# Performance work log

Measured on AMD Instinct MI355X. Metric: run time of the kernel, lower is better.

Reference implementation:

```python
import jax, jax.numpy as jnp
import numpy as np

N = 12000   # nodes (multiple of 120)
E = 192000  # edges
T = 120     # utterances per dialogue
IN = 192
OUT = 6


def _edge_softmax(logits, dst, n):
    # logits: [E, H] -> softmax over incoming edges of each dst node
    m = jax.ops.segment_max(logits, dst, num_segments=n)
    ex = jnp.exp(logits - m[dst])
    s = jax.ops.segment_sum(ex, dst, num_segments=n)
    return ex / s[dst]


def _gatv2(h, src, dst, Wsrc, bsrc, Wdst, bdst, attn, Wres, n):
    # DGL GATv2Conv: e = attn . leakyrelu(fc_src(h)[u] + fc_dst(h)[v]), residual, relu activation
    Hh, F = attn.shape
    fs = (h @ Wsrc + bsrc).reshape(n, Hh, F)
    fd = (h @ Wdst + bdst).reshape(n, Hh, F)
    e = jax.nn.leaky_relu(fs[src] + fd[dst], 0.2)          # [E, H, F]
    logits = jnp.einsum('ehf,hf->eh', e, attn)              # [E, H]
    alpha = _edge_softmax(logits, dst, n)                   # [E, H]
    out = jax.ops.segment_sum(alpha[:, :, None] * fs[src], dst, num_segments=n)
    res = (h @ Wres).reshape(n, Hh, F)
    return jax.nn.relu(out + res)                           # [N, H, F]


def _lstm_dir(x, Wih, Whh, bih, bhh, reverse):
    # x: [T, B, D]; torch gate order i, f, g, o
    B = x.shape[1]
    hid = Whh.shape[1]
    def step(carry, xt):
        h, c = carry
        z = xt @ Wih.T + h @ Whh.T + bih + bhh
        i, f, g, o = jnp.split(z, 4, axis=-1)
        c = jax.nn.sigmoid(f) * c + jax.nn.sigmoid(i) * jnp.tanh(g)
        h = jax.nn.sigmoid(o) * jnp.tanh(c)
        return (h, c), h
    init = (jnp.zeros((B, hid), x.dtype), jnp.zeros((B, hid), x.dtype))
    _, hs = jax.lax.scan(step, init, x, reverse=reverse)
    return hs


def setup_inputs() -> dict:
    key = jax.random.key(0)
    ks = iter(jax.random.split(key, 64))
    def rn(shape, s=0.05):
        return jax.random.normal(next(ks), shape, jnp.float32) * s
    inp = {
        'text': rn((N, 1024), 1.0),
        'audio': rn((N, 512), 1.0),
        'vision': rn((N, 1024), 1.0),
        'edge_src': jax.random.randint(next(ks), (E,), 0, N, jnp.int32),
        'edge_dst': jax.random.randint(next(ks), (E,), 0, N, jnp.int32),
        # modality encoders
        'W_audio': rn((512, 64)), 'b_audio': jnp.zeros((64,), jnp.float32),
        'W_vision': rn((1024, 64)), 'b_vision': jnp.zeros((64,), jnp.float32),
        'W_text': rn((1024, 64)), 'b_text': jnp.zeros((64,), jnp.float32),
        # bidirectional LSTM (hidden=4 -> 16 gate rows)
        'Wih_f': rn((16, IN)), 'Whh_f': rn((16, 4)), 'bih_f': jnp.zeros((16,), jnp.float32), 'bhh_f': jnp.zeros((16,), jnp.float32),
        'Wih_b': rn((16, IN)), 'Whh_b': rn((16, 4)), 'bih_b': jnp.zeros((16,), jnp.float32), 'bhh_b': jnp.zeros((16,), jnp.float32),
        # imputation GraphConv (192->192, norm='both')
        'W_gc': rn((IN, IN)), 'b_gc': jnp.zeros((IN,), jnp.float32),
        # gat2 (cross-modal multi-head GAT, 192 -> 16 heads x 4)
        'Wsrc2': rn((IN, 64)), 'bsrc2': jnp.zeros((64,), jnp.float32),
        'Wdst2': rn((IN, 64)), 'bdst2': jnp.zeros((64,), jnp.float32),
        'attn2': rn((16, 4)), 'Wres2': rn((IN, 64)),
        # gat1 layer 0 (192 -> 16 heads x 32)
        'Wsrc0': rn((IN, 512)), 'bsrc0': jnp.zeros((512,), jnp.float32),
        'Wdst0': rn((IN, 512)), 'bdst0': jnp.zeros((512,), jnp.float32),
        'attn0': rn((16, 32)), 'Wres0': rn((IN, 512)),
        # gat1 layer 1 (512 -> 16 heads x 4)
        'Wsrc1': rn((512, 64)), 'bsrc1': jnp.zeros((64,), jnp.float32),
        'Wdst1': rn((512, 64)), 'bdst1': jnp.zeros((64,), jnp.float32),
        'attn1': rn((16, 4)), 'Wres1': rn((512, 64)),
        # final classifier Linear(136, out_size)
        'W_lin': rn((136, OUT)), 'b_lin': jnp.zeros((OUT,), jnp.float32),
    }
    return inp


def reference(text, audio, vision, edge_src, edge_dst,
              W_audio, b_audio, W_vision, b_vision, W_text, b_text,
              Wih_f, Whh_f, bih_f, bhh_f, Wih_b, Whh_b, bih_b, bhh_b,
              W_gc, b_gc,
              Wsrc2, bsrc2, Wdst2, bdst2, attn2, Wres2,
              Wsrc0, bsrc0, Wdst0, bdst0, attn0, Wres0,
              Wsrc1, bsrc1, Wdst1, bdst1, attn1, Wres1,
              W_lin, b_lin):
    n = text.shape[0]
    # modality encoders (dropout is identity at inference)
    t = text @ W_text + b_text
    a = audio @ W_audio + b_audio
    v = vision @ W_vision + b_vision
    stackFT = jnp.concatenate([t, a, v], axis=1)            # [N, 192]

    # bidirectional LSTM over dialogues of length T=120
    x = stackFT.reshape(-1, T, IN).transpose(1, 0, 2)       # [T, B, 192]
    hf = _lstm_dir(x, Wih_f, Whh_f, bih_f, bhh_f, False)
    hb = _lstm_dir(x, Wih_b, Whh_b, bih_b, bhh_b, True)
    newFeature = jnp.concatenate([hf, hb], -1).transpose(1, 0, 2).reshape(n, 8)

    # GraphConv imputation, norm='both' (degrees clamped to 1 as in DGL)
    ones = jnp.ones((edge_src.shape[0],), stackFT.dtype)
    deg_out = jnp.maximum(jax.ops.segment_sum(ones, edge_src, num_segments=n), 1.0)
    deg_in = jnp.maximum(jax.ops.segment_sum(ones, edge_dst, num_segments=n), 1.0)
    hw = (stackFT @ W_gc) * (deg_out ** -0.5)[:, None]
    h1 = jax.ops.segment_sum(hw[edge_src], edge_dst, num_segments=n) * (deg_in ** -0.5)[:, None] + b_gc
    h = 0.5 * (stackFT + h1)
    # F.normalize(h, p=1)
    h = h / jnp.maximum(jnp.sum(jnp.abs(h), axis=1, keepdims=True), 1e-12)

    # cross-modal multi-head GAT branch -> [N, 64]
    h3 = _gatv2(h, edge_src, edge_dst, Wsrc2, bsrc2, Wdst2, bdst2, attn2, Wres2, n).reshape(n, -1)

    # stacked GATv2 layers
    h = _gatv2(h, edge_src, edge_dst, Wsrc0, bsrc0, Wdst0, bdst0, attn0, Wres0, n).reshape(n, -1)  # [N, 512]
    h = _gatv2(h, edge_src, edge_dst, Wsrc1, bsrc1, Wdst1, bdst1, attn1, Wres1, n).reshape(n, -1)  # [N, 64]

    out = jnp.concatenate([h, newFeature, h3], axis=1) @ W_lin + b_lin  # [N, out_size]
    return out
```

## Files before the change

### kernel.cpp

```cpp
#include <hip/hip_runtime.h>

typedef __attribute__((ext_vector_type(8))) short short8;
typedef __attribute__((ext_vector_type(4))) float f32x4;
typedef _Float16 half8v __attribute__((ext_vector_type(8)));

__device__ __forceinline__ unsigned short f2bf(float f) {
    unsigned u = __float_as_uint(f);
    u += 0x7FFFu + ((u >> 16) & 1u);
    return (unsigned short)(u >> 16);
}
__device__ __forceinline__ float bf2f(unsigned short h) {
    return __uint_as_float((unsigned)h << 16);
}

template<int MF, int OUTMODE>
__global__ __launch_bounds__(256)
void gemm_v7(const unsigned short* __restrict__ A, const unsigned short* __restrict__ B,
             const float* __restrict__ bias, const float* __restrict__ rowscale,
             void* __restrict__ Cv, const float* __restrict__ fin_num,
             const float* __restrict__ fin_den,
             int M, int Nb, int K, int ldc)
{
    __shared__ alignas(16) unsigned short As[MF * 64 * 32];
    __shared__ alignas(16) unsigned short Bs[4 * 64 * 8];
    const int t = threadIdx.x;
    const int w = t >> 6, l = t & 63;
    const int r16 = l & 15, kg = l >> 4;
    const int row0 = blockIdx.x * (64 * MF);
    const int col0 = blockIdx.y * 64;
    const int bcol = t & 63, bkg = t >> 6;

    f32x4 acc[MF][4] = {};
    const short8 z8 = {0, 0, 0, 0, 0, 0, 0, 0};

    int srow[MF], sch[MF];
    bool va[MF];
    const unsigned short* aptr[MF];
#pragma unroll
    for (int it = 0; it < MF; ++it) {
        int idx = it * 256 + t;
        srow[it] = idx >> 2; sch[it] = idx & 3;
        int gm = row0 + srow[it];
        va[it] = gm < M;
        aptr[it] = A + (size_t)gm * K + sch[it] * 8;
    }
    const unsigned short* bptr = B + (size_t)(bkg * 8) * Nb + col0 + bcol;

    short8 pa[MF];
    unsigned short pbv[8];
#pragma unroll
    for (int it = 0; it < MF; ++it)
        pa[it] = va[it] ? *reinterpret_cast<const short8*>(aptr[it]) : z8;
#pragma unroll
    for (int j = 0; j < 8; ++j) pbv[j] = bptr[(size_t)j * Nb];

    for (int k0 = 0; k0 < K; k0 += 32) {
#pragma unroll
        for (int it = 0; it < MF; ++it)
            *reinterpret_cast<short8*>(&As[srow[it] * 32 + sch[it] * 8]) = pa[it];
        {
            short8 hv;
#pragma unroll
            for (int j = 0; j < 8; ++j) hv[j] = (short)pbv[j];
            *reinterpret_cast<short8*>(&Bs[bkg * 512 + bcol * 8]) = hv;
        }
        __syncthreads();
        if (k0 + 32 < K) {
#pragma unroll
            for (int it = 0; it < MF; ++it)
                pa[it] = va[it] ? *reinterpret_cast<const short8*>(aptr[it] + k0 + 32) : z8;
#pragma unroll
            for (int j = 0; j < 8; ++j) pbv[j] = bptr[(size_t)(k0 + 32 + j) * Nb];
        }
        short8 af[MF];
#pragma unroll
        for (int mi = 0; mi < MF; ++mi)
            af[mi] = *reinterpret_cast<const short8*>(&As[((w * MF + mi) * 16 + r16) * 32 + kg * 8]);
#pragma unroll
        for (int ni = 0; ni < 4; ++ni) {
            short8 bf = *reinterpret_cast<const short8*>(&Bs[kg * 512 + (ni * 16 + r16) * 8]);
#pragma unroll
            for (int mi = 0; mi < MF; ++mi)
                acc[mi][ni] = __builtin_amdgcn_mfma_f32_16x16x32_bf16(af[mi], bf, acc[mi][ni], 0, 0, 0);
        }
        __syncthreads();
    }
#pragma unroll
    for (int mi = 0; mi < MF; ++mi)
#pragma unroll
        for (int ni = 0; ni < 4; ++ni) {
            int col = col0 + ni * 16 + r16;
            float bv = bias ? bias[col] : 0.f;
#pragma unroll
            for (int r = 0; r < 4; ++r) {
                int gm = row0 + (w * MF + mi) * 16 + kg * 4 + r;
                if (gm < M) {
                    float val = acc[mi][ni][r] + bv;
                    if (rowscale) val *= rowscale[gm];
                    size_t idx = (size_t)gm * ldc + col;
                    if (OUTMODE == 0) {
                        ((float*)Cv)[idx] = val;
                    } else if (OUTMODE == 1) {
                        ((unsigned short*)Cv)[idx] = f2bf(val);
                    } else {
                        float d = fin_den[(size_t)gm * 16 + (col >> 5)];
                        float inv = (d > 0.f) ? __fdividef(1.f, d) : 0.f;
                        float o = fmaxf(fin_num[idx] * inv + val, 0.f);
                        ((unsigned short*)Cv)[idx] = f2bf(o);
                    }
                }
            }
        }
}

__global__ __launch_bounds__(256)
void enc_f16v6(const float* __restrict__ text, const float* __restrict__ audio, const float* __restrict__ vision,
               const _Float16* __restrict__ Wf16,
               const float* __restrict__ bt, const float* __restrict__ ba, const float* __restrict__ bv,
               float* __restrict__ Cf, unsigned short* __restrict__ Cb, int M)
{
    __shared__ float tbuf[4][16][68];
    const int gw = (blockIdx.x * blockDim.x + threadIdx.x) >> 6;
    const int wib = threadIdx.x >> 6;
    const int l = threadIdx.x & 63;
    const int tpm = M >> 4;
    if (gw >= 3 * tpm) return;
    const int z = gw / tpm;
    const int tidx = gw - z * tpm;
    const float* A  = (z == 0) ? text : (z == 1) ? audio : vision;
    const _Float16* Wp = Wf16 + ((z == 0) ? 0 : (z == 1) ? 65536 : 98304) + l * 8;
    const float* bb = (z == 0) ? bt : (z == 1) ? ba : bv;
    const int KC = (z == 1) ? 16 : 32;

    const float* ap = A + (size_t)(tidx * 16 + (l & 15)) * (KC * 32) + (l >> 4) * 8;

    f32x4 acc0 = {}, acc1 = {}, acc2 = {}, acc3 = {};
    float4 na0 = *reinterpret_cast<const float4*>(ap);
    float4 na1 = *reinterpret_cast<const float4*>(ap + 4);
    half8v nb0 = *reinterpret_cast<const half8v*>(Wp);
    half8v nb1 = *reinterpret_cast<const half8v*>(Wp + 512);
    half8v nb2 = *reinterpret_cast<const half8v*>(Wp + 1024);
    half8v nb3 = *reinterpret_cast<const half8v*>(Wp + 1536);

    for (int kc = 0; kc < KC; ++kc) {
        float4 ca0 = na0, ca1 = na1;
        half8v cb0 = nb0, cb1 = nb1, cb2 = nb2, cb3 = nb3;
        if (kc + 1 < KC) {
            const float* apn = ap + (kc + 1) * 32;
            na0 = *reinterpret_cast<const float4*>(apn);
            na1 = *reinterpret_cast<const float4*>(apn + 4);
            const _Float16* wpn = Wp + (size_t)(kc + 1) * 2048;
            nb0 = *reinterpret_cast<const half8v*>(wpn);
            nb1 = *reinterpret_cast<const half8v*>(wpn + 512);
            nb2 = *reinterpret_cast<const half8v*>(wpn + 1024);
            nb3 = *reinterpret_cast<const half8v*>(wpn + 1536);
        }
        half8v af;
        af[0] = (_Float16)ca0.x; af[1] = (_Float16)ca0.y;
        af[2] = (_Float16)ca0.z; af[3] = (_Float16)ca0.w;
        af[4] = (_Float16)ca1.x; af[5] = (_Float16)ca1.y;
        af[6] = (_Float16)ca1.z; af[7] = (_Float16)ca1.w;
        acc0 = __builtin_amdgcn_mfma_f32_16x16x32_f16(af, cb0, acc0, 0, 0, 0);
        acc1 = __builtin_amdgcn_mfma_f32_16x16x32_f16(af, cb1, acc1, 0, 0, 0);
        acc2 = __builtin_amdgcn_mfma_f32_16x16x32_f16(af, cb2, acc2, 0, 0, 0);
        acc3 = __builtin_amdgcn_mfma_f32_16x16x32_f16(af, cb3, acc3, 0, 0, 0);
    }

    const int r16 = l & 15, hi = l >> 4;
    float* tl = &tbuf[wib][0][0];
#pragma unroll
    for (int cg = 0; cg < 4; ++cg) {
        f32x4 a = (cg == 0) ? acc0 : (cg == 1) ? acc1 : (cg == 2) ? acc2 : acc3;
        int col = cg * 16 + r16;
        float bvv = bb[col];
#pragma unroll
        for (int r = 0; r < 4; ++r)
            tl[(hi * 4 + r) * 68 + col] = a[r] + bvv;
    }
#pragma unroll
    for (int r = 0; r < 16; ++r) {
        float val = tl[r * 68 + l];
        size_t idx = (size_t)(tidx * 16 + r) * 192 + z * 64 + l;
        Cf[idx] = val;
        Cb[idx] = f2bf(val);
    }
}

__global__ void pack_all(const float* __restrict__ Wt, const float* __restrict__ Wa, const float* __restrict__ Wv,
                         const float* __restrict__ Wgc,
                         const float* __restrict__ Ws2, const float* __restrict__ Wd2, const float* __restrict__ Wr2,
                         const float* __restrict__ bs2, const float* __restrict__ bd2,
                         const float* __restrict__ Ws0, const float* __restrict__ Wd0,
                         const float* __restrict__ bs0, const float* __restrict__ bd0,
                         const float* __restrict__ Wr0,
                         const float* __restrict__ Ws1, const float* __restrict__ Wd1, const float* __restrict__ Wr1,
                         const float* __restrict__ bs1, const float* __restrict__ bd1,
                         _Float16* __restrict__ encW, unsigned short* __restrict__ Wall, float* __restrict__ ball)
{
    int gid = blockIdx.x * blockDim.x + threadIdx.x;
    if (gid < 163840) {
        const float* Wsrcp;
        int base;
        if (gid < 65536)      { base = 0;     Wsrcp = Wt; }
        else if (gid < 98304) { base = 65536; Wsrcp = Wa; }
        else                  { base = 98304; Wsrcp = Wv; }
        int i = gid - base;
        int kc = i >> 11, r = i & 2047;
        int cg = r >> 9, lane = (r >> 3) & 63, j = r & 7;
        int k = kc * 32 + (lane >> 4) * 8 + j;
        int col = cg * 16 + (lane & 15);
        encW[gid] = (_Float16)Wsrcp[k * 64 + col];
    }
    if (gid < 36864) {
        Wall[gid] = f2bf(Wgc[gid]);
    } else if (gid < 73728) {
        int i = gid - 36864, k = i / 192, c = i - k * 192;
        float v = (c < 64) ? Ws2[k * 64 + c] : (c < 128) ? Wd2[k * 64 + c - 64] : Wr2[k * 64 + c - 128];
        Wall[gid] = f2bf(v);
    } else if (gid < 270336) {
        int i = gid - 73728, k = i >> 10, c = i & 1023;
        float v = (c < 512) ? Ws0[k * 512 + c] : Wd0[k * 512 + c - 512];
        Wall[gid] = f2bf(v);
    } else if (gid < 368640) {
        Wall[gid] = f2bf(Wr0[gid - 270336]);
    } else if (gid < 466944) {
        int i = gid - 368640, k = i / 192, c = i - k * 192;
        float v = (c < 64) ? Ws1[k * 64 + c] : (c < 128) ? Wd1[k * 64 + c - 64] : Wr1[k * 64 + c - 128];
        Wall[gid] = f2bf(v);
    } else if (gid < 468352) {
        int i = gid - 466944;
        float v;
        if (i < 192)       v = (i < 64) ? bs2[i] : (i < 128) ? bd2[i - 64] : 0.f;
        else if (i < 1216) { int j = i - 192; v = (j < 512) ? bs0[j] : bd0[j - 512]; }
        else               { int j = i - 1216; v = (j < 64) ? bs1[j] : (j < 128) ? bd1[j - 64] : 0.f; }
        ball[i] = v;
    }
}

__global__ void deg_kernel(const int* __restrict__ src, const int* __restrict__ dst,
                           int* degout, int* degin, int E)
{
    int e = blockIdx.x * blockDim.x + threadIdx.x;
    if (e < E) {
        atomicAdd(&degout[src[e]], 1);
        atomicAdd(&degin[dst[e]], 1);
    }
}

__global__ __launch_bounds__(1024)
void scan_kernel(const int* __restrict__ degin, const int* __restrict__ degout,
                 int* __restrict__ rowstart, float* __restrict__ rso, float* __restrict__ rsi, int n)
{
    __shared__ int part[1024];
    int t = threadIdx.x;
    int chunk = (n + 1023) / 1024;
    int s = 0;
    for (int i = 0; i < chunk; ++i) {
        int idx = t * chunk + i;
        if (idx < n) s += degin[idx];
    }
    part[t] = s;
    __syncthreads();
    for (int o = 1; o < 1024; o <<= 1) {
        int v = (t >= o) ? part[t - o] : 0;
        __syncthreads();
        part[t] += v;
        __syncthreads();
    }
    int run = (t > 0) ? part[t - 1] : 0;
    for (int i = 0; i < chunk; ++i) {
        int idx = t * chunk + i;
        if (idx < n) {
            rowstart[idx] = run; run += degin[idx];
            rso[idx] = rsqrtf((float)max(degout[idx], 1));
            rsi[idx] = rsqrtf((float)max(degin[idx], 1));
        }
    }
    if (t == 1023) rowstart[n] = part[1023];
}

__global__ void perm_kernel(const int* __restrict__ dst, const int* __restrict__ rowstart,
                            int* cursor, int* __restrict__ perm, int E)
{
    int e = blockIdx.x * blockDim.x + threadIdx.x;
    if (e < E) {
        int v = dst[e];
        int p = atomicAdd(&cursor[v], 1);
        perm[rowstart[v] + p] = e;
    }
}

__global__ void gather_src_kernel(const int* __restrict__ esrc, int* perm, int E)
{
    int i = blockIdx.x * blockDim.x + threadIdx.x;
    if (i < E) perm[i] = esrc[perm[i]];
}

__global__ void lstm_pre(const float* __restrict__ x, const float* __restrict__ Wf,
                         const float* __restrict__ Wb,
                         const float* bf1, const float* bf2, const float* bb1, const float* bb2,
                         float* __restrict__ xWf, float* __restrict__ xWb, int n)
{
    int gid = blockIdx.x * blockDim.x + threadIdx.x;
    if (gid >= n * 32) return;
    int nn = gid >> 5, r = gid & 31, d = r >> 4, j = r & 15;
    const float* W = (d ? Wb : Wf) + j * 192;
    const float* xr = x + (size_t)nn * 192;
    float s = 0.f;
#pragma unroll 4
    for (int k = 0; k < 192; k += 4) {
        float4 xv = *reinterpret_cast<const float4*>(xr + k);
        float4 wv = *reinterpret_cast<const float4*>(W + k);
        s += xv.x * wv.x + xv.y * wv.y + xv.z * wv.z + xv.w * wv.w;
    }
    s += d ? (bb1[j] + bb2[j]) : (bf1[j] + bf2[j]);
    int b = nn / 120, tt = nn - b * 120;
    (d ? xWb : xWf)[((size_t)b * 16 + j) * 120 + tt] = s;
}

__device__ __forceinline__ float fsigm(float x) { return __fdividef(1.f, 1.f + __expf(-x)); }
__device__ __forceinline__ float ftanh(float x) { return 1.f - __fdividef(2.f, __expf(2.f * x) + 1.f); }

template<int DIR>
__device__ void lstm_chain(const float* __restrict__ xw, const float* __restrict__ whh,
                           float* __restrict__ newF, int b)
{
    int j = threadIdx.x & 15;
    int k = j & 3;
    float4 w = *reinterpret_cast<const float4*>(whh + j * 4);
    const float* xp = xw + ((size_t)b * 16 + j) * 120;
    float h0 = 0.f, h1 = 0.f, h2 = 0.f, h3 = 0.f, cst = 0.f;
    int tb0 = DIR ? 108 : 0;
    float4 a0 = *reinterpret_cast<const float4*>(xp + tb0);
    float4 a1 = *reinterpret_cast<const float4*>(xp + tb0 + 4);
    float4 a2 = *reinterpret_cast<const float4*>(xp + tb0 + 8);
    for (int ch = 0; ch < 10; ++ch) {
        float4 b0 = a0, b1 = a1, b2 = a2;
        if (ch < 9) {
            int nt = DIR ? (96 - ch * 12) : (12 + ch * 12);
            b0 = *reinterpret_cast<const float4*>(xp + nt);
            b1 = *reinterpret_cast<const float4*>(xp + nt + 4);
            b2 = *reinterpret_cast<const float4*>(xp + nt + 8);
        }
        float zz[12] = {a0.x, a0.y, a0.z, a0.w, a1.x, a1.y, a1.z, a1.w, a2.x, a2.y, a2.z, a2.w};
        int tbase = DIR ? (108 - ch * 12) : (ch * 12);
#pragma unroll
        for (int ii = 0; ii < 12; ++ii) {
            int idx = DIR ? (11 - ii) : ii;
            float z = zz[idx] + ((w.x * h0 + w.y * h1) + (w.z * h2 + w.w * h3));
            float zi = __shfl(z, k, 16);
            float zf = __shfl(z, k + 4, 16);
            float zg = __shfl(z, k + 8, 16);
            float zo = __shfl(z, k + 12, 16);
            float ig = fsigm(zi), fg = fsigm(zf), gg = ftanh(zg), og = fsigm(zo);
            cst = fg * cst + ig * gg;
            float hn = og * ftanh(cst);
            h0 = __shfl(hn, 0, 16); h1 = __shfl(hn, 1, 16);
            h2 = __shfl(hn, 2, 16); h3 = __shfl(hn, 3, 16);
            if (j < 4) newF[((size_t)b * 120 + tbase + idx) * 8 + DIR * 4 + j] = hn;
        }
        a0 = b0; a1 = b1; a2 = b2;
    }
}

__global__ __launch_bounds__(64)
void lstm_seq2(const float* __restrict__ xWf, const float* __restrict__ xWb,
               const float* __restrict__ Whhf, const float* __restrict__ Whhb,
               float* __restrict__ newF, int B)
{
    int sub = threadIdx.x >> 4;
    int chain = blockIdx.x * 4 + sub;
    if (chain >= 2 * B) return;
    int d = chain / B;
    int b = chain - d * B;
    if (d == 0) lstm_chain<0>(xWf, Whhf, newF, b);
    else        lstm_chain<1>(xWb, Whhb, newF, b);
}

__global__ __launch_bounds__(256)
void gc_combine5(const float* __restrict__ stackFT, const unsigned short* __restrict__ hw,
                 const int* __restrict__ rowstart, const int* __restrict__ csrc,
                 const float* __restrict__ rs_in,
                 const float* __restrict__ b_gc, unsigned short* __restrict__ hB, int n)
{
    int v = blockIdx.x * 4 + (threadIdx.x >> 6);
    int l = threadIdx.x & 63;
    if (v >= n) return;
    int s0 = rowstart[v], s1 = rowstart[v + 1];
    float sum0 = 0.f, sum1 = 0.f, sum2 = 0.f;

    unsigned short a0 = 0, a1 = 0, a2 = 0, b0 = 0, b1 = 0, b2 = 0;
    auto LD = [&](int i, unsigned short& x0, unsigned short& x1, unsigned short& x2) {
        const unsigned short* hr = hw + (size_t)csrc[i] * 192 + l;
        x0 = hr[0]; x1 = hr[64]; x2 = hr[128];
    };
    int i = s0;
    if (i < s1) LD(i, a0, a1, a2);
    if (i + 1 < s1) LD(i + 1, b0, b1, b2);
    for (; i + 2 < s1; i += 2) {
        unsigned short n0, n1, n2, m0 = 0, m1 = 0, m2 = 0;
        LD(i + 2, n0, n1, n2);
        if (i + 3 < s1) LD(i + 3, m0, m1, m2);
        sum0 += bf2f(a0) + bf2f(b0);
        sum1 += bf2f(a1) + bf2f(b1);
        sum2 += bf2f(a2) + bf2f(b2);
        a0 = n0; a1 = n1; a2 = n2; b0 = m0; b1 = m1; b2 = m2;
    }
    if (i < s1) { sum0 += bf2f(a0); sum1 += bf2f(a1); sum2 += bf2f(a2); }
    if (i + 1 < s1) { sum0 += bf2f(b0); sum1 += bf2f(b1); sum2 += bf2f(b2); }

    float ri = rs_in[v];
    const float* sf = stackFT + (size_t)v * 192 + l;
    float v0 = 0.5f * (sf[0]   + sum0 * ri + b_gc[l]);
    float v1 = 0.5f * (sf[64]  + sum1 * ri + b_gc[l + 64]);
    float v2 = 0.5f * (sf[128] + sum2 * ri + b_gc[l + 128]);
    float r = fabsf(v0) + fabsf(v1) + fabsf(v2);
#pragma unroll
    for (int o = 32; o; o >>= 1) r += __shfl_xor(r, o);
    float inv = __fdividef(1.f, fmaxf(r, 1e-12f));
    unsigned short* hp = hB + (size_t)v * 192 + l;
    hp[0]   = f2bf(v0 * inv);
    hp[64]  = f2bf(v1 * inv);
    hp[128] = f2bf(v2 * inv);
}

__global__ __launch_bounds__(256)
void gat_edge4c(const unsigned short* __restrict__ base,
                const float* __restrict__ attn,
                const int* __restrict__ rowstart, const int* __restrict__ csrc,
                float* __restrict__ outp, int n)
{
    int v = blockIdx.x * 16 + (threadIdx.x >> 4);
    int l = threadIdx.x & 15;
    if (v >= n) return;
    float4 at = *reinterpret_cast<const float4*>(attn + l * 4);
    ushort4 fdu = *reinterpret_cast<const ushort4*>(base + (size_t)v * 192 + 64 + l * 4);
    float fd0 = bf2f(fdu.x), fd1 = bf2f(fdu.y), fd2 = bf2f(fdu.z), fd3 = bf2f(fdu.w);
    float ac0 = 0.f, ac1 = 0.f, ac2 = 0.f, ac3 = 0.f, dn = 0.f;
    int s0 = rowstart[v], s1 = rowstart[v + 1];

    auto LD = [&](int i) -> ushort4 {
        return *reinterpret_cast<const ushort4*>(base + (size_t)csrc[i] * 192 + l * 4);
    };
    auto ACC = [&](ushort4 su) {
        float s0f = bf2f(su.x), s1f = bf2f(su.y), s2f = bf2f(su.z), s3f = bf2f(su.w);
        float e0 = s0f + fd0; e0 = fmaxf(e0, 0.2f * e0);
        float e1 = s1f + fd1; e1 = fmaxf(e1, 0.2f * e1);
        float e2 = s2f + fd2; e2 = fmaxf(e2, 0.2f * e2);
        float e3 = s3f + fd3; e3 = fmaxf(e3, 0.2f * e3);
        float p = e0 * at.x + e1 * at.y + e2 * at.z + e3 * at.w;
        float ex = __expf(p);
        ac0 += ex * s0f; ac1 += ex * s1f; ac2 += ex * s2f; ac3 += ex * s3f;
        dn += ex;
    };
    const ushort4 zu = make_ushort4(0, 0, 0, 0);
    ushort4 c0 = zu, c1 = zu;
    int i = s0;
    if (i < s1) c0 = LD(i);
    if (i + 1 < s1) c1 = LD(i + 1);
    for (; i + 2 < s1; i += 2) {
        ushort4 n0 = LD(i + 2);
        ushort4 n1 = (i + 3 < s1) ? LD(i + 3) : zu;
        ACC(c0); ACC(c1);
        c0 = n0; c1 = n1;
    }
    if (i < s1) ACC(c0);
    if (i + 1 < s1) ACC(c1);

    ushort4 ru = *reinterpret_cast<const ushort4*>(base + (size_t)v * 192 + 128 + l * 4);
    float inv = (dn > 0.f) ? __fdividef(1.f, dn) : 0.f;
    float4 o;
    o.x = fmaxf(ac0 * inv + bf2f(ru.x), 0.f);
    o.y = fmaxf(ac1 * inv + bf2f(ru.y), 0.f);
    o.z = fmaxf(ac2 * inv + bf2f(ru.z), 0.f);
    o.w = fmaxf(ac3 * inv + bf2f(ru.w), 0.f);
    *reinterpret_cast<float4*>(outp + (size_t)v * 64 + l * 4) = o;
}

__global__ __launch_bounds__(256)
void gat_edge32b(const unsigned short* __restrict__ base,
                 const float* __restrict__ attn,
                 const int* __restrict__ rowstart, const int* __restrict__ csrc,
                 float* __restrict__ num, float* __restrict__ den, int n)
{
    int v = blockIdx.x * 4 + (threadIdx.x >> 6);
    int l = threadIdx.x & 63;
    if (v >= n) return;
    float at[8];
    {
        float4 aA = *reinterpret_cast<const float4*>(attn + l * 8);
        float4 aB = *reinterpret_cast<const float4*>(attn + l * 8 + 4);
        at[0] = aA.x; at[1] = aA.y; at[2] = aA.z; at[3] = aA.w;
        at[4] = aB.x; at[5] = aB.y; at[6] = aB.z; at[7] = aB.w;
    }
    float fd[8];
    {
        short8 fdu = *reinterpret_cast<const short8*>(base + (size_t)v * 1024 + 512 + l * 8);
#pragma unroll
        for (int j = 0; j < 8; ++j) fd[j] = bf2f((unsigned short)fdu[j]);
    }
    float acc[8] = {};
    float dn = 0.f;
    int s0 = rowstart[v], s1 = rowstart[v + 1];

    auto LD = [&](int i) -> short8 {
        return *reinterpret_cast<const short8*>(base + (size_t)csrc[i] * 1024 + l * 8);
    };
    auto ACC = [&](short8 su) {
        float sf[8];
        float p = 0.f;
#pragma unroll
        for (int j = 0; j < 8; ++j) {
            sf[j] = bf2f((unsigned short)su[j]);
            float e = sf[j] + fd[j];
            e = fmaxf(e, 0.2f * e);
            p += e * at[j];
        }
        p += __shfl_xor(p, 1, 4);
        p += __shfl_xor(p, 2, 4);
        float ex = __expf(p);
#pragma unroll
        for (int j = 0; j < 8; ++j) acc[j] += ex * sf[j];
        dn += ex;
    };
    const short8 z8 = {0, 0, 0, 0, 0, 0, 0, 0};
    short8 c0 = z8, c1 = z8;
    int i = s0;
    if (i < s1) c0 = LD(i);
    if (i + 1 < s1) c1 = LD(i + 1);
    for (; i + 2 < s1; i += 2) {
        short8 n0 = LD(i + 2);
        short8 n1 = (i + 3 < s1) ? LD(i + 3) : z8;
        ACC(c0); ACC(c1);
        c0 = n0; c1 = n1;
    }
    if (i < s1) ACC(c0);
    if (i + 1 < s1) ACC(c1);

    float* np = num + (size_t)v * 512 + l * 8;
    *reinterpret_cast<float4*>(np)     = make_float4(acc[0], acc[1], acc[2], acc[3]);
    *reinterpret_cast<float4*>(np + 4) = make_float4(acc[4], acc[5], acc[6], acc[7]);
    if ((l & 3) == 0) den[(size_t)v * 16 + (l >> 2)] = dn;
}

__global__ void final_lin(const float* __restrict__ h1, const float* __restrict__ newF,
                          const float* __restrict__ h3, const float* __restrict__ W,
                          const float* __restrict__ bias, float* __restrict__ out, int n)
{
    int gid = blockIdx.x * blockDim.x + threadIdx.x;
    if (gid >= n * 6) return;
    int v = gid / 6, o = gid - v * 6;
    float s = bias[o];
    const float* a = h1 + (size_t)v * 64;
#pragma unroll 8
    for (int r = 0; r < 64; ++r) s += a[r] * W[r * 6 + o];
    const float* b = newF + (size_t)v * 8;
#pragma unroll
    for (int r = 0; r < 8; ++r) s += b[r] * W[(64 + r) * 6 + o];
    const float* c = h3 + (size_t)v * 64;
#pragma unroll 8
    for (int r = 0; r < 64; ++r) s += c[r] * W[(72 + r) * 6 + o];
    out[gid] = s;
}

extern "C" void kernel_launch(void* const* d_in, const int* in_sizes, int n_in,
                              void* d_out, int out_size, void* d_ws, size_t ws_size,
                              hipStream_t stream)
{
    const float* text   = (const float*)d_in[0];
    const float* audio  = (const float*)d_in[1];
    const float* vision = (const float*)d_in[2];
    const int*   esrc   = (const int*)d_in[3];
    const int*   edst   = (const int*)d_in[4];
    const float* W_audio = (const float*)d_in[5];  const float* b_audio = (const float*)d_in[6];
    const float* W_vision= (const float*)d_in[7];  const float* b_vision= (const float*)d_in[8];
    const float* W_text  = (const float*)d_in[9];  const float* b_text  = (const float*)d_in[10];
    const float* Wih_f = (const float*)d_in[11]; const float* Whh_f = (const float*)d_in[12];
    const float* bih_f = (const float*)d_in[13]; const float* bhh_f = (const float*)d_in[14];
    const float* Wih_b = (const float*)d_in[15]; const float* Whh_b = (const float*)d_in[16];
    const float* bih_b = (const float*)d_in[17]; const float* bhh_b = (const float*)d_in[18];
    const float* W_gc  = (const float*)d_in[19]; const float* b_gc  = (const float*)d_in[20];
    const float* Wsrc2 = (const float*)d_in[21]; const float* bsrc2 = (const float*)d_in[22];
    const float* Wdst2 = (const float*)d_in[23]; const float* bdst2 = (const float*)d_in[24];
    const float* attn2 = (const float*)d_in[25]; const float* Wres2 = (const float*)d_in[26];
    const float* Wsrc0 = (const float*)d_in[27]; const float* bsrc0 = (const float*)d_in[28];
    const float* Wdst0 = (const float*)d_in[29]; const float* bdst0 = (const float*)d_in[30];
    const float* attn0 = (const float*)d_in[31]; const float* Wres0 = (const float*)d_in[32];
    const float* Wsrc1 = (const float*)d_in[33]; const float* bsrc1 = (const float*)d_in[34];
    const float* Wdst1 = (const float*)d_in[35]; const float* bdst1 = (const float*)d_in[36];
    const float* attn1 = (const float*)d_in[37]; const float* Wres1 = (const float*)d_in[38];
    const float* W_lin = (const float*)d_in[39]; const float* b_lin = (const float*)d_in[40];
    float* out = (float*)d_out;

    const int n = in_sizes[0] / 1024;
    const int E = in_sizes[3];
    const int B = n / 120;

    char* p = (char*)d_ws;
    auto alloc_f = [&](size_t cnt) { float* r = (float*)p; p += ((cnt * 4 + 255) / 256) * 256; return r; };
    auto alloc_h = [&](size_t cnt) { unsigned short* r = (unsigned short*)p; p += ((cnt * 2 + 255) / 256) * 256; return r; };
    auto alloc_i = [&](size_t cnt) { int* r = (int*)p; p += ((cnt * 4 + 255) / 256) * 256; return r; };
    float*          stackFT = alloc_f((size_t)n * 192);
    unsigned short* stackBF = alloc_h((size_t)n * 192);
    unsigned short* hbufBF  = alloc_h((size_t)n * 192);
    unsigned short* encW    = alloc_h(163840);
    float* xWf     = alloc_f((size_t)n * 16);
    float* xWb     = alloc_f((size_t)n * 16);
    float* newF    = alloc_f((size_t)n * 8);
    float* big0    = alloc_f((size_t)n * 512);
    float* big1    = alloc_f((size_t)n * 512);
    float* big2    = alloc_f((size_t)n * 512);
    float* den     = alloc_f((size_t)n * 16);
    float* h3      = alloc_f((size_t)n * 64);
    float* h1s     = alloc_f((size_t)n * 64);
    float* rs_out  = alloc_f(n);
    float* rs_in   = alloc_f(n);
    int* zero_base = alloc_i((size_t)3 * n);
    int* degout = zero_base;
    int* degin  = zero_base + n;
    int* cursor = zero_base + 2 * n;
    int* rowstart = alloc_i((size_t)n + 1);
    int* perm     = alloc_i((size_t)E);
    if ((size_t)(p - (char*)d_ws) > ws_size) return;

    unsigned short* Wall = (unsigned short*)h1s;
    float* ball = h1s + 240000;
    const unsigned short* Wp_gc = Wall;
    const unsigned short* Wp_g2 = Wall + 36864;
    const unsigned short* Wp_g0 = Wall + 73728;
    const unsigned short* Wp_r0 = Wall + 270336;
    const unsigned short* Wp_g1 = Wall + 368640;
    const float* bp_g2 = ball;
    const float* bp_g0 = ball + 192;
    const float* bp_g1 = ball + 1216;

    hipMemsetAsync(zero_base, 0, (size_t)3 * n * 4, stream);
    pack_all<<<(468352 + 255) / 256, 256, 0, stream>>>(
        W_text, W_audio, W_vision, W_gc,
        Wsrc2, Wdst2, Wres2, bsrc2, bdst2,
        Wsrc0, Wdst0, bsrc0, bdst0, Wres0,
        Wsrc1, Wdst1, Wres1, bsrc1, bdst1,
        (_Float16*)encW, Wall, ball);
    deg_kernel<<<(E + 255) / 256, 256, 0, stream>>>(esrc, edst, degout, degin, E);
    scan_kernel<<<1, 1024, 0, stream>>>(degin, degout, rowstart, rs_out, rs_in, n);
    perm_kernel<<<(E + 255) / 256, 256, 0, stream>>>(edst, rowstart, cursor, perm, E);
    gather_src_kernel<<<(E + 255) / 256, 256, 0, stream>>>(esrc, perm, E);
    const int* csrc = perm;

    auto gemm = [&](auto mf_tag, auto om_tag, const unsigned short* A, const unsigned short* Bm,
                    const float* bias, const float* rsc, void* Cp,
                    const float* fnum, const float* fden, int M, int Nb, int K, int ldc) {
        constexpr int MF = decltype(mf_tag)::value;
        constexpr int OM = decltype(om_tag)::value;
        dim3 grid((M + 64 * MF - 1) / (64 * MF), Nb / 64);
        gemm_v7<MF, OM><<<grid, 256, 0, stream>>>(A, Bm, bias, rsc, Cp, fnum, fden, M, Nb, K, ldc);
    };
    using I1 = std::integral_constant<int, 1>;
    using I2 = std::integral_constant<int, 2>;
    using O1 = std::integral_constant<int, 1>;
    using O2 = std::integral_constant<int, 2>;

    {
        int waves = 3 * (n >> 4);
        enc_f16v6<<<(waves * 64 + 255) / 256, 256, 0, stream>>>(
            text, audio, vision, (const _Float16*)encW,
            b_text, b_audio, b_vision, stackFT, stackBF, n);
    }

    lstm_pre<<<(n * 32 + 255) / 256, 256, 0, stream>>>(stackFT, Wih_f, Wih_b,
                                                       bih_f, bhh_f, bih_b, bhh_b, xWf, xWb, n);
    lstm_seq2<<<(2 * B + 3) / 4, 64, 0, stream>>>(xWf, xWb, Whh_f, Whh_b, newF, B);

    gemm(I1{}, O1{}, stackBF, Wp_gc, nullptr, rs_out, big0, nullptr, nullptr, n, 192, 192, 192);
    gc_combine5<<<(n + 3) / 4, 256, 0, stream>>>(stackFT, (const unsigned short*)big0,
                                                 rowstart, csrc, rs_in, b_gc, hbufBF, n);

    gemm(I1{}, O1{}, hbufBF, Wp_g2, bp_g2, nullptr, big0, nullptr, nullptr, n, 192, 192, 192);
    gat_edge4c<<<(n + 15) / 16, 256, 0, stream>>>((const unsigned short*)big0, attn2, rowstart, csrc, h3, n);

    gemm(I2{}, O1{}, hbufBF, Wp_g0, bp_g0, nullptr, big0, nullptr, nullptr, n, 1024, 192, 1024);
    gat_edge32b<<<(n + 3) / 4, 256, 0, stream>>>((const unsigned short*)big0, attn0, rowstart, csrc, big2, den, n);
    gemm(I1{}, O2{}, hbufBF, Wp_r0, nullptr, nullptr, big1, big2, den, n, 512, 192, 512);

    gemm(I1{}, O1{}, (const unsigned short*)big1, Wp_g1, bp_g1, nullptr, big0, nullptr, nullptr, n, 192, 512, 192);
    gat_edge4c<<<(n + 15) / 16, 256, 0, stream>>>((const unsigned short*)big0, attn1, rowstart, csrc, h1s, n);

    final_lin<<<(n * 6 + 255) / 256, 256, 0, stream>>>(h1s, newF, h3, W_lin, b_lin, out, n);
}
```

Baseline: 357.9 us.

## Move LSTM input projection onto bf16 MFMA GEMM and deepen edge-loop prefetch

Replaces the scalar fp32 lstm_pre kernel with the existing bf16 MFMA GEMM path. This adds a packed, zero-padded 64-column weight block and a new output mode that scatters results into the transposed per-dialogue xWf/xWb layout. Separately, the GAT edge aggregation loops now prefetch four edges per iteration instead of two, to hide more gather latency. The LSTM input is now bf16 rather than fp32, which loses some precision, and half of the padded GEMM columns are wasted work.

```diff
diff --git a/kernel.cpp b/kernel.cpp
--- a/kernel.cpp
+++ b/kernel.cpp
@@ -102,11 +102,18 @@
                         ((float*)Cv)[idx] = val;
                     } else if (OUTMODE == 1) {
                         ((unsigned short*)Cv)[idx] = f2bf(val);
-                    } else {
+                    } else if (OUTMODE == 2) {
                         float d = fin_den[(size_t)gm * 16 + (col >> 5)];
                         float inv = (d > 0.f) ? __fdividef(1.f, d) : 0.f;
                         float o = fmaxf(fin_num[idx] * inv + val, 0.f);
                         ((unsigned short*)Cv)[idx] = f2bf(o);
+                    } else {
+                        if (col < 32) {
+                            int d = col >> 4, j = col & 15;
+                            int bb = gm / 120, tt = gm - bb * 120;
+                            float* dst = d ? (float*)fin_num : (float*)Cv;
+                            dst[((size_t)bb * 16 + j) * 120 + tt] = val;
+                        }
                     }
                 }
             }
@@ -195,6 +202,9 @@
                          const float* __restrict__ Wr0,
                          const float* __restrict__ Ws1, const float* __restrict__ Wd1, const float* __restrict__ Wr1,
                          const float* __restrict__ bs1, const float* __restrict__ bd1,
+                         const float* __restrict__ Wihf, const float* __restrict__ Wihb,
+                         const float* __restrict__ bihf, const float* __restrict__ bhhf,
+                         const float* __restrict__ bihb, const float* __restrict__ bhhb,
                          _Float16* __restrict__ encW, unsigned short* __restrict__ Wall, float* __restrict__ ball)
 {
     int gid = blockIdx.x * blockDim.x + threadIdx.x;
@@ -227,12 +237,17 @@
         int i = gid - 368640, k = i / 192, c = i - k * 192;
         float v = (c < 64) ? Ws1[k * 64 + c] : (c < 128) ? Wd1[k * 64 + c - 64] : Wr1[k * 64 + c - 128];
         Wall[gid] = f2bf(v);
-    } else if (gid < 468352) {
-        int i = gid - 466944;
+    } else if (gid < 479232) {
+        int i = gid - 466944, k = i >> 6, c = i & 63;
+        float v = (c < 16) ? Wihf[c * 192 + k] : (c < 32) ? Wihb[(c - 16) * 192 + k] : 0.f;
+        Wall[gid] = f2bf(v);
+    } else if (gid < 480672) {
+        int i = gid - 479232;
         float v;
         if (i < 192)       v = (i < 64) ? bs2[i] : (i < 128) ? bd2[i - 64] : 0.f;
         else if (i < 1216) { int j = i - 192; v = (j < 512) ? bs0[j] : bd0[j - 512]; }
-        else               { int j = i - 1216; v = (j < 64) ? bs1[j] : (j < 128) ? bd1[j - 64] : 0.f; }
+        else if (i < 1408) { int j = i - 1216; v = (j < 64) ? bs1[j] : (j < 128) ? bd1[j - 64] : 0.f; }
+        else               { int j = i - 1408; v = (j < 16) ? (bihf[j] + bhhf[j]) : (bihb[j - 16] + bhhb[j - 16]); }
         ball[i] = v;
     }
 }
@@ -294,28 +309,6 @@
 {
     int i = blockIdx.x * blockDim.x + threadIdx.x;
     if (i < E) perm[i] = esrc[perm[i]];
-}
-
-__global__ void lstm_pre(const float* __restrict__ x, const float* __restrict__ Wf,
-                         const float* __restrict__ Wb,
-                         const float* bf1, const float* bf2, const float* bb1, const float* bb2,
-                         float* __restrict__ xWf, float* __restrict__ xWb, int n)
-{
-    int gid = blockIdx.x * blockDim.x + threadIdx.x;
-    if (gid >= n * 32) return;
-    int nn = gid >> 5, r = gid & 31, d = r >> 4, j = r & 15;
-    const float* W = (d ? Wb : Wf) + j * 192;
-    const float* xr = x + (size_t)nn * 192;
-    float s = 0.f;
-#pragma unroll 4
-    for (int k = 0; k < 192; k += 4) {
-        float4 xv = *reinterpret_cast<const float4*>(xr + k);
-        float4 wv = *reinterpret_cast<const float4*>(W + k);
-        s += xv.x * wv.x + xv.y * wv.y + xv.z * wv.z + xv.w * wv.w;
-    }
-    s += d ? (bb1[j] + bb2[j]) : (bf1[j] + bf2[j]);
-    int b = nn / 120, tt = nn - b * 120;
-    (d ? xWb : xWf)[((size_t)b * 16 + j) * 120 + tt] = s;
 }
 
 __device__ __forceinline__ float fsigm(float x) { return __fdividef(1.f, 1.f + __expf(-x)); }
@@ -454,18 +447,24 @@
         dn += ex;
     };
     const ushort4 zu = make_ushort4(0, 0, 0, 0);
-    ushort4 c0 = zu, c1 = zu;
+    ushort4 c0 = zu, c1 = zu, c2 = zu, c3 = zu;
     int i = s0;
-    if (i < s1) c0 = LD(i);
+    if (i     < s1) c0 = LD(i);
     if (i + 1 < s1) c1 = LD(i + 1);
-    for (; i + 2 < s1; i += 2) {
-        ushort4 n0 = LD(i + 2);
-        ushort4 n1 = (i + 3 < s1) ? LD(i + 3) : zu;
-        ACC(c0); ACC(c1);
-        c0 = n0; c1 = n1;
-    }
-    if (i < s1) ACC(c0);
+    if (i + 2 < s1) c2 = LD(i + 2);
+    if (i + 3 < s1) c3 = LD(i + 3);
+    for (; i + 4 < s1; i += 4) {
+        ushort4 n0 = LD(i + 4);
+        ushort4 n1 = (i + 5 < s1) ? LD(i + 5) : zu;
+        ushort4 n2 = (i + 6 < s1) ? LD(i + 6) : zu;
+        ushort4 n3 = (i + 7 < s1) ? LD(i + 7) : zu;
+        ACC(c0); ACC(c1); ACC(c2); ACC(c3);
+        c0 = n0; c1 = n1; c2 = n2; c3 = n3;
+    }
+    if (i     < s1) ACC(c0);
     if (i + 1 < s1) ACC(c1);
+    if (i + 2 < s1) ACC(c2);
+    if (i + 3 < s1) ACC(c3);
 
     ushort4 ru = *reinterpret_cast<const ushort4*>(base + (size_t)v * 192 + 128 + l * 4);
     float inv = (dn > 0.f) ? __fdividef(1.f, dn) : 0.f;
@@ -524,18 +523,24 @@
         dn += ex;
     };
     const short8 z8 = {0, 0, 0, 0, 0, 0, 0, 0};
-    short8 c0 = z8, c1 = z8;
+    short8 c0 = z8, c1 = z8, c2 = z8, c3 = z8;
     int i = s0;
-    if (i < s1) c0 = LD(i);
+    if (i     < s1) c0 = LD(i);
     if (i + 1 < s1) c1 = LD(i + 1);
-    for (; i + 2 < s1; i += 2) {
-        short8 n0 = LD(i + 2);
-        short8 n1 = (i + 3 < s1) ? LD(i + 3) : z8;
-        ACC(c0); ACC(c1);
-        c0 = n0; c1 = n1;
-    }
-    if (i < s1) ACC(c0);
+    if (i + 2 < s1) c2 = LD(i + 2);
+    if (i + 3 < s1) c3 = LD(i + 3);
+    for (; i + 4 < s1; i += 4) {
+        short8 n0 = LD(i + 4);
+        short8 n1 = (i + 5 < s1) ? LD(i + 5) : z8;
+        short8 n2 = (i + 6 < s1) ? LD(i + 6) : z8;
+        short8 n3 = (i + 7 < s1) ? LD(i + 7) : z8;
+        ACC(c0); ACC(c1); ACC(c2); ACC(c3);
+        c0 = n0; c1 = n1; c2 = n2; c3 = n3;
+    }
+    if (i     < s1) ACC(c0);
     if (i + 1 < s1) ACC(c1);
+    if (i + 2 < s1) ACC(c2);
+    if (i + 3 < s1) ACC(c3);
 
     float* np = num + (size_t)v * 512 + l * 8;
     *reinterpret_cast<float4*>(np)     = make_float4(acc[0], acc[1], acc[2], acc[3]);
@@ -625,21 +630,24 @@
 
     unsigned short* Wall = (unsigned short*)h1s;
     float* ball = h1s + 240000;
-    const unsigned short* Wp_gc = Wall;
-    const unsigned short* Wp_g2 = Wall + 36864;
-    const unsigned short* Wp_g0 = Wall + 73728;
-    const unsigned short* Wp_r0 = Wall + 270336;
-    const unsigned short* Wp_g1 = Wall + 368640;
-    const float* bp_g2 = ball;
-    const float* bp_g0 = ball + 192;
-    const float* bp_g1 = ball + 1216;
+    const unsigned short* Wp_gc   = Wall;
+    const unsigned short* Wp_g2   = Wall + 36864;
+    const unsigned short* Wp_g0   = Wall + 73728;
+    const unsigned short* Wp_r0   = Wall + 270336;
+    const unsigned short* Wp_g1   = Wall + 368640;
+    const unsigned short* Wp_lstm = Wall + 466944;
+    const float* bp_g2   = ball;
+    const float* bp_g0   = ball + 192;
+    const float* bp_g1   = ball + 1216;
+    const float* bp_lstm = ball + 1408;
 
     hipMemsetAsync(zero_base, 0, (size_t)3 * n * 4, stream);
-    pack_all<<<(468352 + 255) / 256, 256, 0, stream>>>(
+    pack_all<<<(480672 + 255) / 256, 256, 0, stream>>>(
         W_text, W_audio, W_vision, W_gc,
         Wsrc2, Wdst2, Wres2, bsrc2, bdst2,
         Wsrc0, Wdst0, bsrc0, bdst0, Wres0,
         Wsrc1, Wdst1, Wres1, bsrc1, bdst1,
+        Wih_f, Wih_b, bih_f, bhh_f, bih_b, bhh_b,
         (_Float16*)encW, Wall, ball);
     deg_kernel<<<(E + 255) / 256, 256, 0, stream>>>(esrc, edst, degout, degin, E);
     scan_kernel<<<1, 1024, 0, stream>>>(degin, degout, rowstart, rs_out, rs_in, n);
@@ -659,6 +667,7 @@
     using I2 = std::integral_constant<int, 2>;
     using O1 = std::integral_constant<int, 1>;
     using O2 = std::integral_constant<int, 2>;
+    using O3 = std::integral_constant<int, 3>;
 
     {
         int waves = 3 * (n >> 4);
@@ -667,8 +676,7 @@
             b_text, b_audio, b_vision, stackFT, stackBF, n);
     }
 
-    lstm_pre<<<(n * 32 + 255) / 256, 256, 0, stream>>>(stackFT, Wih_f, Wih_b,
-                                                       bih_f, bhh_f, bih_b, bhh_b, xWf, xWb, n);
+    gemm(I1{}, O3{}, stackBF, Wp_lstm, bp_lstm, nullptr, xWf, xWb, nullptr, n, 64, 192, 64);
     lstm_seq2<<<(2 * B + 3) / 4, 64, 0, stream>>>(xWf, xWb, Whh_f, Whh_b, newF, B);
 
     gemm(I1{}, O1{}, stackBF, Wp_gc, nullptr, rs_out, big0, nullptr, nullptr, n, 192, 192, 192);
```

Measured after the change: 331.4 us. 1.08x faster.
